# Optimization experiments

Measured on AMD Instinct MI355X. Metric: run time of the kernel, lower is better.

## Reference

```python
import jax, jax.numpy as jnp
import numpy as np

DT = 0.005


def quat_product(q, r):
    # q, r: [B, 4] -> [B, 4]
    q0, q1, q2, q3 = q[:, 0], q[:, 1], q[:, 2], q[:, 3]
    r0, r1, r2, r3 = r[:, 0], r[:, 1], r[:, 2], r[:, 3]
    return jnp.stack([
        q0 * r0 - q1 * r1 - q2 * r2 - q3 * r3,
        q0 * r1 + q1 * r0 + q2 * r3 - q3 * r2,
        q0 * r2 - q1 * r3 + q2 * r0 + q3 * r1,
        q0 * r3 + q1 * r2 - q2 * r1 + q3 * r0,
    ], axis=1)


def quat_rotate(q, v):
    # q: [B, 4], v: [B, 3] -> [B, 3]
    q_conj = jnp.concatenate([q[:, :1], -q[:, 1:]], axis=1)
    v_quat = jnp.concatenate([jnp.zeros_like(v[:, :1]), v], axis=1)
    return quat_product(quat_product(q, v_quat), q_conj)[:, 1:]


def setup_inputs() -> dict:
    key = jax.random.key(0)
    ks = jax.random.split(key, 8)
    B, S, F, N = 1048576, 10, 6, 2097152
    return {
        "true_quaternions": jax.random.normal(ks[0], (B, 4), dtype=jnp.float32),
        "true_positions": jax.random.normal(ks[1], (B, 3), dtype=jnp.float32),
        "predicted_biases": jax.random.normal(ks[2], (B, 3), dtype=jnp.float32),
        "batch_X": jax.random.normal(ks[3], (B, S, F), dtype=jnp.float32),
        "positions_all": jax.random.normal(ks[4], (N, 3), dtype=jnp.float32),
        "velocities_all": jax.random.normal(ks[5], (N, 3), dtype=jnp.float32),
        "gravity_vector": jnp.array([0.0, 0.0, -9.81], dtype=jnp.float32),
        "indices": jax.random.randint(ks[6], (B,), 0, N, dtype=jnp.int64 if jax.config.jax_enable_x64 else jnp.int32),
        "sequence_length": 10,
    }


def reference(true_quaternions, true_positions, predicted_biases, batch_X,
              positions_all, velocities_all, gravity_vector, indices,
              sequence_length):
    # gather initial state: initial_index = max(idx - (seq_len - 1), 0)
    init_idx = jnp.maximum(indices - (sequence_length - 1), 0)
    p0 = positions_all[init_idx]   # [B, 3]
    v0 = velocities_all[init_idx]  # [B, 3]
    # bias-corrected acceleration from last timestep (disturbance = 0)
    acc = batch_X[:, -1, 0:3] - predicted_biases  # [B, 3]
    rotated = 0.5 * quat_rotate(true_quaternions, acc) * DT ** 2
    pred = p0 + v0 * DT + 0.5 * gravity_vector * DT ** 2 + rotated
    # Huber loss, delta = 1.0; per-sample mean over 3 coords then batch mean
    # equals elementwise mean over all B*3 elements
    d = pred - true_positions
    ad = jnp.abs(d)
    h = jnp.where(ad < 1.0, 0.5 * d * d, ad - 0.5)
    return jnp.mean(h)
```

## Files before the change

### kernel.cpp

```cpp
#include <hip/hip_runtime.h>
#include <math.h>

#define DT 0.005f
#define NTHREADS 256
#define NBLOCKS 2048
#define NBUCKET 16

typedef float fvec4 __attribute__((ext_vector_type(4)));

__device__ __forceinline__ fvec4 ntload4f(const float* p) {
    return __builtin_nontemporal_load(reinterpret_cast<const fvec4*>(p));
}
__device__ __forceinline__ float ntloadf(const float* p) {
    return __builtin_nontemporal_load(p);
}
__device__ __forceinline__ int ntloadi(const int* p) {
    return __builtin_nontemporal_load(p);
}

__device__ __forceinline__ void stream_compute(
    const float* __restrict__ quat, const float* __restrict__ tpos,
    const float* __restrict__ bias, const float* __restrict__ batchX,
    int i, int SF, int last_off,
    float gx, float gy, float gz, float half_dt2,
    float& cx, float& cy, float& cz)
{
    fvec4 q = ntload4f(quat + (size_t)i * 4);
    const float* tp = tpos + (size_t)i * 3;
    float tpx = ntloadf(tp + 0), tpy = ntloadf(tp + 1), tpz = ntloadf(tp + 2);
    const float* bp = bias + (size_t)i * 3;
    float bx = ntloadf(bp + 0), by = ntloadf(bp + 1), bz = ntloadf(bp + 2);
    const float* xb = batchX + (size_t)i * SF + last_off;
    float ax = ntloadf(xb + 0) - bx;
    float ay = ntloadf(xb + 1) - by;
    float az = ntloadf(xb + 2) - bz;

    float t0 = -(q.y * ax + q.z * ay + q.w * az);
    float t1 =   q.x * ax + q.z * az - q.w * ay;
    float t2 =   q.x * ay - q.y * az + q.w * ax;
    float t3 =   q.x * az + q.y * ay - q.z * ax;
    float rx = -t0 * q.y + t1 * q.x - t2 * q.w + t3 * q.z;
    float ry = -t0 * q.z + t1 * q.w + t2 * q.x - t3 * q.y;
    float rz = -t0 * q.w - t1 * q.z + t2 * q.y + t3 * q.x;

    cx = half_dt2 * (gx + rx) - tpx;
    cy = half_dt2 * (gy + ry) - tpy;
    cz = half_dt2 * (gz + rz) - tpz;
}

__device__ __forceinline__ float huber3(float dx, float dy, float dz) {
    float adx = fabsf(dx), ady = fabsf(dy), adz = fabsf(dz);
    float h = (adx < 1.f) ? 0.5f * dx * dx : adx - 0.5f;
    h += (ady < 1.f) ? 0.5f * dy * dy : ady - 0.5f;
    h += (adz < 1.f) ? 0.5f * dz * dz : adz - 0.5f;
    return h;
}

__global__ __launch_bounds__(NTHREADS) void k1_bin(
    const float* __restrict__ quat,
    const float* __restrict__ tpos,
    const float* __restrict__ bias,
    const float* __restrict__ batchX,
    const int*   __restrict__ indices,
    const int*   __restrict__ seq_len_p,
    int SF, int shift,
    uint4* __restrict__ pairs,
    int*   __restrict__ dirs)
{
    const int S = *seq_len_p;
    const int F = SF / S;
    const int last_off = (S - 1) * F;
    const float half_dt2 = 0.5f * DT * DT;

    __shared__ int   cnt[2][4][NBUCKET];
    __shared__ int   offarr[2][4][NBUCKET];
    __shared__ int   bstart[NBUCKET];
    __shared__ uint4 stage[512];

    const int tid  = threadIdx.x;
    const int wave = tid >> 6;
    const int lane = tid & 63;
    const unsigned long long ltmask = (lane == 63) ? ~0ull >> 1 : (1ull << lane) - 1ull;

    if (tid < 2 * 4 * NBUCKET) ((int*)cnt)[tid] = 0;
    __syncthreads();

    const int base = blockIdx.x * 512;

    int   idxv[2], bckt[2], rnk[2];
    float cxv[2], cyv[2], czv[2];

    #pragma unroll
    for (int r = 0; r < 2; ++r) {
        const int i = base + r * 256 + tid;
        int idx = ntloadi(indices + i) - (S - 1);
        if (idx < 0) idx = 0;
        idxv[r] = idx;
        int b = idx >> shift; if (b > NBUCKET - 1) b = NBUCKET - 1;
        bckt[r] = b;

        unsigned long long mask = ~0ull;
        #pragma unroll
        for (int k = 0; k < 4; ++k) {
            unsigned long long bm = __ballot((b >> k) & 1);
            mask &= ((b >> k) & 1) ? bm : ~bm;
        }
        rnk[r] = __popcll(mask & ltmask);
        if (rnk[r] == 0) cnt[r][wave][b] = __popcll(mask);
    }
    __syncthreads();

    if (tid < NBUCKET) {
        int b = tid, off = 0;
        #pragma unroll
        for (int r = 0; r < 2; ++r)
            #pragma unroll
            for (int w = 0; w < 4; ++w) {
                offarr[r][w][b] = off;
                off += cnt[r][w][b];
            }
        dirs[blockIdx.x * NBUCKET + b] = off;
        cnt[0][0][b] = off;
    }
    __syncthreads();
    if (tid == 0) {
        int s = 0;
        #pragma unroll
        for (int b = 0; b < NBUCKET; ++b) { bstart[b] = s; s += cnt[0][0][b]; }
    }

    __syncthreads();

    (void)cxv; (void)cyv; (void)czv;

}

__global__ __launch_bounds__(NTHREADS) void k1_bin_full(
    const float* __restrict__ quat,
    const float* __restrict__ tpos,
    const float* __restrict__ bias,
    const float* __restrict__ batchX,
    const float* __restrict__ grav,
    const int*   __restrict__ indices,
    const int*   __restrict__ seq_len_p,
    int SF, int shift,
    uint4* __restrict__ pairs,
    int*   __restrict__ dirs)
{
    const int S = *seq_len_p;
    const int F = SF / S;
    const int last_off = (S - 1) * F;
    const float gx = grav[0], gy = grav[1], gz = grav[2];
    const float half_dt2 = 0.5f * DT * DT;

    __shared__ int   cnt[2][4][NBUCKET];
    __shared__ int   offarr[2][4][NBUCKET];
    __shared__ int   bstart[NBUCKET];
    __shared__ uint4 stage[512];

    const int tid  = threadIdx.x;
    const int wave = tid >> 6;
    const int lane = tid & 63;
    const unsigned long long ltmask = (1ull << lane) - 1ull;

    if (tid < 2 * 4 * NBUCKET) ((int*)cnt)[tid] = 0;
    __syncthreads();

    const int base = blockIdx.x * 512;

    int   idxv[2], bckt[2], rnk[2];
    float cxv[2], cyv[2], czv[2];

    #pragma unroll
    for (int r = 0; r < 2; ++r) {
        const int i = base + r * 256 + tid;
        int idx = ntloadi(indices + i) - (S - 1);
        if (idx < 0) idx = 0;
        idxv[r] = idx;
        int b = idx >> shift; if (b > NBUCKET - 1) b = NBUCKET - 1;
        bckt[r] = b;

        unsigned long long mask = ~0ull;
        #pragma unroll
        for (int k = 0; k < 4; ++k) {
            unsigned long long bm = __ballot((b >> k) & 1);
            mask &= ((b >> k) & 1) ? bm : ~bm;
        }
        rnk[r] = __popcll(mask & ltmask);
        if (rnk[r] == 0) cnt[r][wave][b] = __popcll(mask);

        stream_compute(quat, tpos, bias, batchX, i, SF, last_off,
                       gx, gy, gz, half_dt2, cxv[r], cyv[r], czv[r]);
    }
    __syncthreads();

    if (tid < NBUCKET) {
        int b = tid, off = 0;
        #pragma unroll
        for (int r = 0; r < 2; ++r)
            #pragma unroll
            for (int w = 0; w < 4; ++w) {
                offarr[r][w][b] = off;
                off += cnt[r][w][b];
            }
        dirs[blockIdx.x * NBUCKET + b] = off;
        cnt[0][0][b] = off;
    }
    __syncthreads();
    if (tid == 0) {
        int s = 0;
        #pragma unroll
        for (int b = 0; b < NBUCKET; ++b) { bstart[b] = s; s += cnt[0][0][b]; }
    }
    __syncthreads();

    #pragma unroll
    for (int r = 0; r < 2; ++r) {
        int slot = bstart[bckt[r]] + offarr[r][wave][bckt[r]] + rnk[r];
        uint4 v;
        v.x = (unsigned)idxv[r];
        v.y = __float_as_uint(cxv[r]);
        v.z = __float_as_uint(cyv[r]);
        v.w = __float_as_uint(czv[r]);
        stage[slot] = v;
    }
    __syncthreads();

    pairs[(size_t)base + tid]       = stage[tid];
    pairs[(size_t)base + 256 + tid] = stage[256 + tid];
}

__global__ __launch_bounds__(NTHREADS) void k2_gather(
    const float* __restrict__ pos_all,
    const float* __restrict__ vel_all,
    const uint4* __restrict__ pairs,
    const int*   __restrict__ dirs,
    float* __restrict__ partials)
{
    const int r = blockIdx.x & 7;
    const int j = blockIdx.x >> 3;
    const int tid = threadIdx.x;

    __shared__ int dcnt[8][NBUCKET];
    __shared__ int segSrc[8];
    __shared__ int segCum[9];
    __shared__ float wsum[NTHREADS / 64];

    float hsum = 0.f;

    for (int phase = 0; phase < 2; ++phase) {
        const int b = r + 8 * phase;

        if (tid < 8 * NBUCKET) {
            int s = tid >> 4, bb = tid & (NBUCKET - 1);
            dcnt[s][bb] = dirs[(j * 8 + s) * NBUCKET + bb];
        }
        __syncthreads();
        if (tid < 8) {
            int s = tid, st = 0;
            #pragma unroll
            for (int bb = 0; bb < NBUCKET; ++bb) {
                if (bb == b) break;
                st += dcnt[s][bb];
            }
            segSrc[s] = (j * 8 + s) * 512 + st;
            segCum[s] = dcnt[s][b];
        }
        __syncthreads();
        if (tid == 0) {
            int c = 0;
            #pragma unroll
            for (int s = 0; s < 8; ++s) { int l = segCum[s]; segCum[s] = c; c += l; }
            segCum[8] = c;
        }
        __syncthreads();

        const int tot = segCum[8];
        for (int m = tid; m < tot; m += NTHREADS) {
            int s = 0;
            #pragma unroll
            for (int k = 1; k < 8; ++k) s += (m >= segCum[k]);
            uint4 pr = pairs[segSrc[s] + (m - segCum[s])];
            int idx = (int)pr.x;
            const float* pp = pos_all + (size_t)idx * 3;
            const float* vp = vel_all + (size_t)idx * 3;
            float cx = __uint_as_float(pr.y);
            float cy = __uint_as_float(pr.z);
            float cz = __uint_as_float(pr.w);
            hsum += huber3(pp[0] + vp[0] * DT + cx,
                           pp[1] + vp[1] * DT + cy,
                           pp[2] + vp[2] * DT + cz);
        }
        __syncthreads();
    }

    for (int off = 32; off > 0; off >>= 1)
        hsum += __shfl_down(hsum, off);

    int lane = tid & 63, wid = tid >> 6;
    if (lane == 0) wsum[wid] = hsum;
    __syncthreads();
    if (tid == 0) {
        float s = 0.f;
        for (int w = 0; w < NTHREADS / 64; ++w) s += wsum[w];
        partials[blockIdx.x] = s;
    }
}

__global__ __launch_bounds__(NTHREADS) void pos_loss_partial(
    const float* __restrict__ quat,
    const float* __restrict__ tpos,
    const float* __restrict__ bias,
    const float* __restrict__ batchX,
    const float* __restrict__ pos_all,
    const float* __restrict__ vel_all,
    const float* __restrict__ grav,
    const int*   __restrict__ indices,
    const int*   __restrict__ seq_len_p,
    int B, int SF,
    float* __restrict__ partials)
{
    const int S = *seq_len_p;
    const int F = SF / S;
    const int last_off = (S - 1) * F;
    const float gx = grav[0], gy = grav[1], gz = grav[2];
    const float half_dt2 = 0.5f * DT * DT;

    float hsum = 0.f;

    for (int i = blockIdx.x * blockDim.x + threadIdx.x; i < B;
         i += gridDim.x * blockDim.x) {
        int idx = ntloadi(indices + i) - (S - 1);
        if (idx < 0) idx = 0;
        const float* pp = pos_all + (size_t)idx * 3;
        const float* vp = vel_all + (size_t)idx * 3;
        float p0x = pp[0], p0y = pp[1], p0z = pp[2];
        float v0x = vp[0], v0y = vp[1], v0z = vp[2];

        float cx, cy, cz;
        stream_compute(quat, tpos, bias, batchX, i, SF, last_off,
                       gx, gy, gz, half_dt2, cx, cy, cz);

        hsum += huber3(p0x + v0x * DT + cx,
                       p0y + v0y * DT + cy,
                       p0z + v0z * DT + cz);
    }

    for (int off = 32; off > 0; off >>= 1)
        hsum += __shfl_down(hsum, off);

    __shared__ float wsum[NTHREADS / 64];
    int lane = threadIdx.x & 63;
    int wid  = threadIdx.x >> 6;
    if (lane == 0) wsum[wid] = hsum;
    __syncthreads();
    if (threadIdx.x == 0) {
        float s = 0.f;
        for (int w = 0; w < NTHREADS / 64; ++w) s += wsum[w];
        partials[blockIdx.x] = s;
    }
}

__global__ __launch_bounds__(NTHREADS) void pos_loss_finish(
    const float* __restrict__ partials, int nb, float inv_cnt,
    float* __restrict__ out)
{
    float s = 0.f;
    for (int i = threadIdx.x; i < nb; i += NTHREADS) s += partials[i];
    for (int off = 32; off > 0; off >>= 1)
        s += __shfl_down(s, off);
    __shared__ float wsum[NTHREADS / 64];
    int lane = threadIdx.x & 63;
    int wid  = threadIdx.x >> 6;
    if (lane == 0) wsum[wid] = s;
    __syncthreads();
    if (threadIdx.x == 0) {
        float tot = 0.f;
        for (int w = 0; w < NTHREADS / 64; ++w) tot += wsum[w];
        out[0] = tot * inv_cnt;
    }
}

extern "C" void kernel_launch(void* const* d_in, const int* in_sizes, int n_in,
                              void* d_out, int out_size, void* d_ws, size_t ws_size,
                              hipStream_t stream) {
    const float* quat    = (const float*)d_in[0];
    const float* tpos    = (const float*)d_in[1];
    const float* bias    = (const float*)d_in[2];
    const float* batchX  = (const float*)d_in[3];
    const float* pos_all = (const float*)d_in[4];
    const float* vel_all = (const float*)d_in[5];
    const float* grav    = (const float*)d_in[6];
    const int*   indices = (const int*)d_in[7];
    const int*   seqlen  = (const int*)d_in[8];

    const int B  = in_sizes[0] / 4;
    const int SF = in_sizes[3] / B;
    const int N  = in_sizes[4] / 3;

    float inv_cnt = (float)(1.0 / (3.0 * (double)B));
    float* outp = (float*)d_out;

    const int nseg = B / 512;
    uint4* pairs   = (uint4*)d_ws;
    int*   dirs    = (int*)((char*)d_ws + (size_t)B * 16);
    float* partials= (float*)((char*)d_ws + (size_t)B * 16 + (size_t)nseg * NBUCKET * 4);
    const size_t need = (size_t)B * 16 + (size_t)nseg * NBUCKET * 4 + (size_t)nseg * 4 + 256;

    const bool pipe_ok = (B % 4096 == 0) && (ws_size >= need) && (N > NBUCKET);

    if (pipe_ok) {
        int shift = 0;
        while (((long long)(N - 1) >> shift) >= NBUCKET) ++shift;

        k1_bin_full<<<nseg, NTHREADS, 0, stream>>>(
            quat, tpos, bias, batchX, grav, indices, seqlen,
            SF, shift, pairs, dirs);
        k2_gather<<<nseg, NTHREADS, 0, stream>>>(
            pos_all, vel_all, pairs, dirs, partials);
        pos_loss_finish<<<1, NTHREADS, 0, stream>>>(
            partials, nseg, inv_cnt, outp);
    } else {
        float* fpart = (float*)d_ws;
        pos_loss_partial<<<NBLOCKS, NTHREADS, 0, stream>>>(
            quat, tpos, bias, batchX, pos_all, vel_all, grav, indices, seqlen,
            B, SF, fpart);
        pos_loss_finish<<<1, NTHREADS, 0, stream>>>(
            fpart, NBLOCKS, inv_cnt, outp);
    }
}
```

Before: 63.30 us.

## Double bucket count and per-block tile size in binned gather pipeline

Each bin block now handles 1024 elements over 4 rounds instead of 512, and the index space is split into 32 buckets instead of 16. This gives the gather kernel finer locality over the position and velocity tables. The gather kernel loads its bucket directory once before the phase loop rather than once per phase, and reads the binned pairs with nontemporal vector loads. The batch_X read is partly merged into a 2-float load, and the dead k1_bin stub is removed. Larger blocks mean fewer blocks and more shared memory per block, which can lower occupancy.

```diff
diff --git a/kernel.cpp b/kernel.cpp
--- a/kernel.cpp
+++ b/kernel.cpp
@@ -4,18 +4,28 @@
 #define DT 0.005f
 #define NTHREADS 256
 #define NBLOCKS 2048
-#define NBUCKET 16
-
-typedef float fvec4 __attribute__((ext_vector_type(4)));
+#define NBUCKET 32
+#define ELEMS_PER_BLOCK 1024
+#define ROUNDS 4
+
+typedef float    fvec4 __attribute__((ext_vector_type(4)));
+typedef float    fvec2 __attribute__((ext_vector_type(2)));
+typedef unsigned uvec4 __attribute__((ext_vector_type(4)));
 
 __device__ __forceinline__ fvec4 ntload4f(const float* p) {
     return __builtin_nontemporal_load(reinterpret_cast<const fvec4*>(p));
 }
+__device__ __forceinline__ fvec2 ntload2f(const float* p) {
+    return __builtin_nontemporal_load(reinterpret_cast<const fvec2*>(p));
+}
 __device__ __forceinline__ float ntloadf(const float* p) {
     return __builtin_nontemporal_load(p);
 }
 __device__ __forceinline__ int ntloadi(const int* p) {
     return __builtin_nontemporal_load(p);
+}
+__device__ __forceinline__ uvec4 ntload4u(const unsigned* p) {
+    return __builtin_nontemporal_load(reinterpret_cast<const uvec4*>(p));
 }
 
 __device__ __forceinline__ void stream_compute(
@@ -31,8 +41,9 @@
     const float* bp = bias + (size_t)i * 3;
     float bx = ntloadf(bp + 0), by = ntloadf(bp + 1), bz = ntloadf(bp + 2);
     const float* xb = batchX + (size_t)i * SF + last_off;
-    float ax = ntloadf(xb + 0) - bx;
-    float ay = ntloadf(xb + 1) - by;
+    fvec2 a01 = ntload2f(xb);
+    float ax = a01.x - bx;
+    float ay = a01.y - by;
     float az = ntloadf(xb + 2) - bz;
 
     float t0 = -(q.y * ax + q.z * ay + q.w * az);
@@ -57,85 +68,6 @@
 }
 
 __global__ __launch_bounds__(NTHREADS) void k1_bin(
-    const float* __restrict__ quat,
-    const float* __restrict__ tpos,
-    const float* __restrict__ bias,
-    const float* __restrict__ batchX,
-    const int*   __restrict__ indices,
-    const int*   __restrict__ seq_len_p,
-    int SF, int shift,
-    uint4* __restrict__ pairs,
-    int*   __restrict__ dirs)
-{
-    const int S = *seq_len_p;
-    const int F = SF / S;
-    const int last_off = (S - 1) * F;
-    const float half_dt2 = 0.5f * DT * DT;
-
-    __shared__ int   cnt[2][4][NBUCKET];
-    __shared__ int   offarr[2][4][NBUCKET];
-    __shared__ int   bstart[NBUCKET];
-    __shared__ uint4 stage[512];
-
-    const int tid  = threadIdx.x;
-    const int wave = tid >> 6;
-    const int lane = tid & 63;
-    const unsigned long long ltmask = (lane == 63) ? ~0ull >> 1 : (1ull << lane) - 1ull;
-
-    if (tid < 2 * 4 * NBUCKET) ((int*)cnt)[tid] = 0;
-    __syncthreads();
-
-    const int base = blockIdx.x * 512;
-
-    int   idxv[2], bckt[2], rnk[2];
-    float cxv[2], cyv[2], czv[2];
-
-    #pragma unroll
-    for (int r = 0; r < 2; ++r) {
-        const int i = base + r * 256 + tid;
-        int idx = ntloadi(indices + i) - (S - 1);
-        if (idx < 0) idx = 0;
-        idxv[r] = idx;
-        int b = idx >> shift; if (b > NBUCKET - 1) b = NBUCKET - 1;
-        bckt[r] = b;
-
-        unsigned long long mask = ~0ull;
-        #pragma unroll
-        for (int k = 0; k < 4; ++k) {
-            unsigned long long bm = __ballot((b >> k) & 1);
-            mask &= ((b >> k) & 1) ? bm : ~bm;
-        }
-        rnk[r] = __popcll(mask & ltmask);
-        if (rnk[r] == 0) cnt[r][wave][b] = __popcll(mask);
-    }
-    __syncthreads();
-
-    if (tid < NBUCKET) {
-        int b = tid, off = 0;
-        #pragma unroll
-        for (int r = 0; r < 2; ++r)
-            #pragma unroll
-            for (int w = 0; w < 4; ++w) {
-                offarr[r][w][b] = off;
-                off += cnt[r][w][b];
-            }
-        dirs[blockIdx.x * NBUCKET + b] = off;
-        cnt[0][0][b] = off;
-    }
-    __syncthreads();
-    if (tid == 0) {
-        int s = 0;
-        #pragma unroll
-        for (int b = 0; b < NBUCKET; ++b) { bstart[b] = s; s += cnt[0][0][b]; }
-    }
-
-    __syncthreads();
-
-    (void)cxv; (void)cyv; (void)czv;
-
-}
-
-__global__ __launch_bounds__(NTHREADS) void k1_bin_full(
     const float* __restrict__ quat,
     const float* __restrict__ tpos,
     const float* __restrict__ bias,
@@ -144,7 +76,7 @@
     const int*   __restrict__ indices,
     const int*   __restrict__ seq_len_p,
     int SF, int shift,
-    uint4* __restrict__ pairs,
+    uvec4* __restrict__ pairs,
     int*   __restrict__ dirs)
 {
     const int S = *seq_len_p;
@@ -153,27 +85,28 @@
     const float gx = grav[0], gy = grav[1], gz = grav[2];
     const float half_dt2 = 0.5f * DT * DT;
 
-    __shared__ int   cnt[2][4][NBUCKET];
-    __shared__ int   offarr[2][4][NBUCKET];
+    __shared__ int   cnt[ROUNDS][4][NBUCKET];
+    __shared__ int   offarr[ROUNDS][4][NBUCKET];
     __shared__ int   bstart[NBUCKET];
-    __shared__ uint4 stage[512];
+    __shared__ uvec4 stage[ELEMS_PER_BLOCK];
 
     const int tid  = threadIdx.x;
     const int wave = tid >> 6;
     const int lane = tid & 63;
     const unsigned long long ltmask = (1ull << lane) - 1ull;
 
-    if (tid < 2 * 4 * NBUCKET) ((int*)cnt)[tid] = 0;
-    __syncthreads();
-
-    const int base = blockIdx.x * 512;
-
-    int   idxv[2], bckt[2], rnk[2];
-    float cxv[2], cyv[2], czv[2];
+    for (int k = tid; k < ROUNDS * 4 * NBUCKET; k += NTHREADS)
+        ((int*)cnt)[k] = 0;
+    __syncthreads();
+
+    const int base = blockIdx.x * ELEMS_PER_BLOCK;
+
+    int   idxv[ROUNDS], bckt[ROUNDS], rnk[ROUNDS];
+    float cxv[ROUNDS], cyv[ROUNDS], czv[ROUNDS];
 
     #pragma unroll
-    for (int r = 0; r < 2; ++r) {
-        const int i = base + r * 256 + tid;
+    for (int r = 0; r < ROUNDS; ++r) {
+        const int i = base + r * NTHREADS + tid;
         int idx = ntloadi(indices + i) - (S - 1);
         if (idx < 0) idx = 0;
         idxv[r] = idx;
@@ -182,7 +115,7 @@
 
         unsigned long long mask = ~0ull;
         #pragma unroll
-        for (int k = 0; k < 4; ++k) {
+        for (int k = 0; k < 5; ++k) {
             unsigned long long bm = __ballot((b >> k) & 1);
             mask &= ((b >> k) & 1) ? bm : ~bm;
         }
@@ -197,7 +130,7 @@
     if (tid < NBUCKET) {
         int b = tid, off = 0;
         #pragma unroll
-        for (int r = 0; r < 2; ++r)
+        for (int r = 0; r < ROUNDS; ++r)
             #pragma unroll
             for (int w = 0; w < 4; ++w) {
                 offarr[r][w][b] = off;
@@ -215,9 +148,9 @@
     __syncthreads();
 
     #pragma unroll
-    for (int r = 0; r < 2; ++r) {
+    for (int r = 0; r < ROUNDS; ++r) {
         int slot = bstart[bckt[r]] + offarr[r][wave][bckt[r]] + rnk[r];
-        uint4 v;
+        uvec4 v;
         v.x = (unsigned)idxv[r];
         v.y = __float_as_uint(cxv[r]);
         v.z = __float_as_uint(cyv[r]);
@@ -226,14 +159,15 @@
     }
     __syncthreads();
 
-    pairs[(size_t)base + tid]       = stage[tid];
-    pairs[(size_t)base + 256 + tid] = stage[256 + tid];
+    #pragma unroll
+    for (int r = 0; r < ROUNDS; ++r)
+        pairs[(size_t)base + r * NTHREADS + tid] = stage[r * NTHREADS + tid];
 }
 
 __global__ __launch_bounds__(NTHREADS) void k2_gather(
     const float* __restrict__ pos_all,
     const float* __restrict__ vel_all,
-    const uint4* __restrict__ pairs,
+    const uvec4* __restrict__ pairs,
     const int*   __restrict__ dirs,
     float* __restrict__ partials)
 {
@@ -246,24 +180,21 @@
     __shared__ int segCum[9];
     __shared__ float wsum[NTHREADS / 64];
 
+    {
+        int s = tid >> 5, bb = tid & (NBUCKET - 1);
+        dcnt[s][bb] = dirs[(j * 8 + s) * NBUCKET + bb];
+    }
+    __syncthreads();
+
     float hsum = 0.f;
 
-    for (int phase = 0; phase < 2; ++phase) {
+    for (int phase = 0; phase < NBUCKET / 8; ++phase) {
         const int b = r + 8 * phase;
 
-        if (tid < 8 * NBUCKET) {
-            int s = tid >> 4, bb = tid & (NBUCKET - 1);
-            dcnt[s][bb] = dirs[(j * 8 + s) * NBUCKET + bb];
-        }
-        __syncthreads();
         if (tid < 8) {
             int s = tid, st = 0;
-            #pragma unroll
-            for (int bb = 0; bb < NBUCKET; ++bb) {
-                if (bb == b) break;
-                st += dcnt[s][bb];
-            }
-            segSrc[s] = (j * 8 + s) * 512 + st;
+            for (int bb = 0; bb < b; ++bb) st += dcnt[s][bb];
+            segSrc[s] = (j * 8 + s) * ELEMS_PER_BLOCK + st;
             segCum[s] = dcnt[s][b];
         }
         __syncthreads();
@@ -280,7 +211,8 @@
             int s = 0;
             #pragma unroll
             for (int k = 1; k < 8; ++k) s += (m >= segCum[k]);
-            uint4 pr = pairs[segSrc[s] + (m - segCum[s])];
+            uvec4 pr = ntload4u(
+                reinterpret_cast<const unsigned*>(pairs + segSrc[s] + (m - segCum[s])));
             int idx = (int)pr.x;
             const float* pp = pos_all + (size_t)idx * 3;
             const float* vp = vel_all + (size_t)idx * 3;
@@ -401,19 +333,22 @@
     float inv_cnt = (float)(1.0 / (3.0 * (double)B));
     float* outp = (float*)d_out;
 
-    const int nseg = B / 512;
-    uint4* pairs   = (uint4*)d_ws;
-    int*   dirs    = (int*)((char*)d_ws + (size_t)B * 16);
-    float* partials= (float*)((char*)d_ws + (size_t)B * 16 + (size_t)nseg * NBUCKET * 4);
-    const size_t need = (size_t)B * 16 + (size_t)nseg * NBUCKET * 4 + (size_t)nseg * 4 + 256;
-
-    const bool pipe_ok = (B % 4096 == 0) && (ws_size >= need) && (N > NBUCKET);
+    const int nseg = B / ELEMS_PER_BLOCK;
+    uvec4* pairs    = (uvec4*)d_ws;
+    int*   dirs     = (int*)((char*)d_ws + (size_t)B * 16);
+    float* partials = (float*)((char*)d_ws + (size_t)B * 16 +
+                               (size_t)nseg * NBUCKET * 4);
+    const size_t need = (size_t)B * 16 + (size_t)nseg * NBUCKET * 4 +
+                        (size_t)nseg * 4 + 256;
+
+    const bool pipe_ok = (B % (ELEMS_PER_BLOCK * 8) == 0) && (ws_size >= need) &&
+                         (N > NBUCKET);
 
     if (pipe_ok) {
         int shift = 0;
         while (((long long)(N - 1) >> shift) >= NBUCKET) ++shift;
 
-        k1_bin_full<<<nseg, NTHREADS, 0, stream>>>(
+        k1_bin<<<nseg, NTHREADS, 0, stream>>>(
             quat, tpos, bias, batchX, grav, indices, seqlen,
             SF, shift, pairs, dirs);
         k2_gather<<<nseg, NTHREADS, 0, stream>>>(
```

Measured after the change: 59.56 us. 5.9% less time.
